# Performance work log

Measured on AMD Instinct MI355X. Metric: run time of the kernel, lower is better.

The kernel has to match this reference:

```python
import jax, jax.numpy as jnp
import numpy as np

C = 128
PC = 6
NH = 8
HD = C // NH
EPS = 1e-5


def _layernorm(x, g, b):
    m = jnp.mean(x, axis=-1, keepdims=True)
    v = jnp.mean((x - m) ** 2, axis=-1, keepdims=True)
    return (x - m) * jax.lax.rsqrt(v + EPS) * g + b


def setup_inputs() -> dict:
    key = jax.random.key(0)
    ks = jax.random.split(key, 16)
    s = 0.02
    inp = {
        "x": jax.random.normal(ks[0], (2, C, 32, 64, 64), dtype=jnp.float32),
        "polar_coords": jax.random.normal(ks[1], (2, PC, 32, 64, 64), dtype=jnp.float32),
        "Wq": jax.random.normal(ks[2], (C, C), dtype=jnp.float32) * s,
        "bq": jnp.zeros((C,), jnp.float32),
        "Wk": jax.random.normal(ks[3], (C, C), dtype=jnp.float32) * s,
        "bk": jnp.zeros((C,), jnp.float32),
        "Wv": jax.random.normal(ks[4], (C, C), dtype=jnp.float32) * s,
        "bv": jnp.zeros((C,), jnp.float32),
        "Wp": jax.random.normal(ks[5], (PC, C), dtype=jnp.float32) * s,
        "bp": jnp.zeros((C,), jnp.float32),
        "Wo": jax.random.normal(ks[6], (C, C), dtype=jnp.float32) * s,
        "bo": jnp.zeros((C,), jnp.float32),
        "g1": jnp.ones((C,), jnp.float32),
        "beta1": jnp.zeros((C,), jnp.float32),
        "g2": jnp.ones((C,), jnp.float32),
        "beta2": jnp.zeros((C,), jnp.float32),
        "W1": jax.random.normal(ks[7], (C, 4 * C), dtype=jnp.float32) * s,
        "bf1": jnp.zeros((4 * C,), jnp.float32),
        "W2": jax.random.normal(ks[8], (4 * C, C), dtype=jnp.float32) * s,
        "bf2": jnp.zeros((C,), jnp.float32),
    }
    return inp


def reference(x, polar_coords, Wq, bq, Wk, bk, Wv, bv, Wp, bp, Wo, bo,
              g1, beta1, g2, beta2, W1, bf1, W2, bf2):
    B, Cc, D, H, W = x.shape
    N = B * D * H * W
    # [B,C,D,H,W] -> [N,C]
    x_flat = jnp.transpose(x, (0, 2, 3, 4, 1)).reshape(N, Cc)
    polar_flat = jnp.transpose(polar_coords, (0, 2, 3, 4, 1)).reshape(N, -1)

    x_with_polar = x_flat + polar_flat @ Wp + bp
    residual = x_with_polar
    x_norm = _layernorm(x_with_polar, g1, beta1)

    Q = (x_norm @ Wq + bq).reshape(N, NH, HD)
    K = (x_norm @ Wk + bk).reshape(N, NH, HD)
    V = (x_norm @ Wv + bv).reshape(N, NH, HD)

    # tiny per-token cross-head attention: scores [N, NH, NH]
    scores = jnp.einsum('nhd,ngd->nhg', Q, K) / np.float32(np.sqrt(HD))
    attn = jax.nn.softmax(scores, axis=-1)
    attended = jnp.einsum('nhg,ngd->nhd', attn, V).reshape(N, Cc)

    out = attended @ Wo + bo + residual
    residual2 = out
    h = _layernorm(out, g2, beta2)
    h = jax.nn.relu(h @ W1 + bf1) @ W2 + bf2
    out = h + residual2

    out = out.reshape(B, D, H, W, Cc)
    return jnp.transpose(out, (0, 4, 1, 2, 3))
```

## Files before the change

kernel.cpp:

```cpp
#include <hip/hip_runtime.h>

typedef unsigned short u16;
typedef float f32x4 __attribute__((ext_vector_type(4)));
typedef short bf16x8 __attribute__((ext_vector_type(8)));

#define DHW 131072
#define OFF_WQ 0
#define OFF_WK 16384
#define OFF_WV 32768
#define OFF_WO 49152
#define OFF_W1 65536
#define OFF_W2 131072

__device__ __forceinline__ float b2f(u16 u){ union{unsigned i; float f;} x; x.i=((unsigned)u)<<16; return x.f; }
__device__ __forceinline__ u16 f2b(float f){ union{float f; unsigned u;} x; x.f=f; unsigned r=x.u+0x7fffu+((x.u>>16)&1u); return (u16)(r>>16); }
__device__ __forceinline__ int cofs(int tok, int cch){ return (tok<<7) + ((((cch>>3) ^ (tok&7)))<<3) + (cch&7); }

__global__ void pack_w(const float* __restrict__ Wq, const float* __restrict__ Wk,
                       const float* __restrict__ Wv, const float* __restrict__ Wo,
                       const float* __restrict__ W1, const float* __restrict__ W2,
                       u16* __restrict__ ws){
  int tid = blockIdx.x*256 + threadIdx.x;
  const float* src; int dst, K, N, fb;
  if      (tid <  2048){ src=Wq; dst=OFF_WQ; K=128; N=128; fb=tid;       }
  else if (tid <  4096){ src=Wk; dst=OFF_WK; K=128; N=128; fb=tid-2048;  }
  else if (tid <  6144){ src=Wv; dst=OFF_WV; K=128; N=128; fb=tid-4096;  }
  else if (tid <  8192){ src=Wo; dst=OFF_WO; K=128; N=128; fb=tid-6144;  }
  else if (tid < 16384){ src=W1; dst=OFF_W1; K=128; N=512; fb=tid-8192;  }
  else                 { src=W2; dst=OFF_W2; K=512; N=128; fb=tid-16384; }
  int l = fb & 63, f = fb >> 6;
  int ksc = K >> 5;
  int nt = f / ksc, ks = f - nt*ksc;
  int k0 = ks*32 + ((l>>4)<<3);
  int col = nt*16 + (l&15);
  union { uint4 v; u16 u[8]; } pk;
  #pragma unroll
  for (int j=0;j<8;j++) pk.u[j] = f2b(src[(k0+j)*N + col]);
  *reinterpret_cast<uint4*>(ws + dst + f*512 + l*8) = pk.v;
}

__device__ __forceinline__ void zacc(f32x4 (&a)[4][2]){
  #pragma unroll
  for (int i=0;i<4;i++){ a[i][0]=(f32x4){0.f,0.f,0.f,0.f}; a[i][1]=(f32x4){0.f,0.f,0.f,0.f}; }
}
__device__ __forceinline__ void mmT(const u16* __restrict__ act, const u16* __restrict__ wf,
                                    int ctb, int ksc, int ks0, int l, f32x4 (&acc)[4][2]){
  #pragma unroll
  for (int ks=0; ks<4; ++ks){
    bf16x8 w0 = *(const bf16x8*)(wf + ((ctb+0)*ksc + ks0+ks)*512 + l*8);
    bf16x8 w1 = *(const bf16x8*)(wf + ((ctb+1)*ksc + ks0+ks)*512 + l*8);
    int g = ks*4 + (l>>4);
    #pragma unroll
    for (int tt=0; tt<4; ++tt){
      int tok = tt*16 + (l&15);
      bf16x8 a = *(const bf16x8*)(act + (tok<<7) + ((g ^ (tok&7))<<3));
      acc[tt][0] = __builtin_amdgcn_mfma_f32_16x16x32_bf16(w0, a, acc[tt][0], 0,0,0);
      acc[tt][1] = __builtin_amdgcn_mfma_f32_16x16x32_bf16(w1, a, acc[tt][1], 0,0,0);
    }
  }
}
__device__ __forceinline__ void packT(ushort4 (&pk)[4][2], const f32x4 (&acc)[4][2],
                                      const u16* __restrict__ bias, int ctb, int l, bool relu){
  #pragma unroll
  for (int cw=0; cw<2; ++cw){
    int cch = (ctb+cw)*16 + ((l>>4)<<2);
    float b0=b2f(bias[cch]), b1=b2f(bias[cch+1]), b2v=b2f(bias[cch+2]), b3=b2f(bias[cch+3]);
    #pragma unroll
    for (int tt=0; tt<4; ++tt){
      float v0=acc[tt][cw][0]+b0, v1=acc[tt][cw][1]+b1, v2=acc[tt][cw][2]+b2v, v3=acc[tt][cw][3]+b3;
      if (relu){ v0=fmaxf(v0,0.f); v1=fmaxf(v1,0.f); v2=fmaxf(v2,0.f); v3=fmaxf(v3,0.f); }
      pk[tt][cw] = (ushort4){ f2b(v0), f2b(v1), f2b(v2), f2b(v3) };
    }
  }
}
__device__ __forceinline__ void storePK(u16* dst, const ushort4 (&pk)[4][2], int ctb, int l){
  #pragma unroll
  for (int cw=0; cw<2; ++cw){
    int cch = ((ctb+cw)*16 + ((l>>4)<<2)) & 127;
    #pragma unroll
    for (int tt=0; tt<4; ++tt){
      int tok = tt*16 + (l&15);
      *(ushort4*)&dst[cofs(tok,cch)] = pk[tt][cw];
    }
  }
}
__device__ __forceinline__ void load16(const u16* buf, int t, int c0, float* o){
  int g = c0 >> 3;
  union { uint4 v; u16 u[8]; } a, b;
  a.v = *(const uint4*)&buf[(t<<7) + (( g    ^ (t&7))<<3)];
  b.v = *(const uint4*)&buf[(t<<7) + (((g+1) ^ (t&7))<<3)];
  #pragma unroll
  for (int j=0;j<8;j++){ o[j]=b2f(a.u[j]); o[8+j]=b2f(b.u[j]); }
}

__global__ __launch_bounds__(256,4) void fused(
    const float* __restrict__ x, const float* __restrict__ pol,
    const float* __restrict__ Wp, const u16* __restrict__ ws,
    const float* __restrict__ bp, const float* __restrict__ bq,
    const float* __restrict__ bk, const float* __restrict__ bv,
    const float* __restrict__ bo, const float* __restrict__ bf1,
    const float* __restrict__ bf2, const float* __restrict__ g1,
    const float* __restrict__ be1, const float* __restrict__ g2,
    const float* __restrict__ be2, float* __restrict__ out)
{
  __shared__ __align__(16) unsigned char arena[40448];
  u16*   bufA = (u16*)  (arena);
  u16*   bufB = (u16*)  (arena + 16384);
  float* red   = (float*)(arena + 32768);
  float* stats = (float*)(arena + 34816);
  u16*   par   = (u16*)  (arena + 35328);

  const int tid = threadIdx.x;
  const int t   = tid & 63;
  const int p   = __builtin_amdgcn_readfirstlane(tid >> 6);
  const int l   = t;

  for (int i=tid; i<2560; i+=256){
    float v;
    if      (i< 128) v = bp [i];
    else if (i< 256) v = g1 [i-128];
    else if (i< 384) v = be1[i-256];
    else if (i< 512) v = g2 [i-384];
    else if (i< 640) v = be2[i-512];
    else if (i<1408) v = Wp [i-640];
    else if (i<1536) v = bq [i-1408];
    else if (i<1664) v = bk [i-1536];
    else if (i<1792) v = bv [i-1664];
    else if (i<1920) v = bo [i-1792];
    else if (i<2048) v = bf2[i-1920];
    else             v = bf1[i-2048];
    par[i] = f2b(v);
  }
  const int bi   = (int)((blockIdx.x*64) >> 17);
  const int dhw0 = (int)((blockIdx.x*64) & (DHW-1));
  const float* xb = x   + (size_t)bi*128*DHW + dhw0;
  const float* pb = pol + (size_t)bi*6*DHW + dhw0;
  float pl6[6];
  #pragma unroll
  for (int j=0;j<6;j++) pl6[j] = pb[(size_t)j*DHW + t];
  __syncthreads();

  float xp[32]; float s1=0.f, s2=0.f;
  #pragma unroll
  for (int it=0; it<32; ++it){
    int c = p*32 + it;
    float a = xb[(size_t)c*DHW + t] + b2f(par[c]);
    #pragma unroll
    for (int j=0;j<6;j++) a = fmaf(pl6[j], b2f(par[640 + j*128 + c]), a);
    xp[it]=a; s1+=a; s2+=a*a;
  }
  #pragma unroll
  for (int cl=0; cl<4; ++cl){
    union { uint4 v; u16 u[8]; } pk;
    #pragma unroll
    for (int j=0;j<8;j++) pk.u[j]=f2b(xp[cl*8+j]);
    *(uint4*)&bufB[(t<<7) + (((p*4+cl) ^ (t&7))<<3)] = pk.v;
  }
  red[p*64+t]=s1; red[256+p*64+t]=s2;
  __syncthreads();
  if (tid < 64){
    float a=0.f,b=0.f;
    #pragma unroll
    for (int i=0;i<4;i++){ a+=red[i*64+tid]; b+=red[256+i*64+tid]; }
    float m=a*0.0078125f, v=b*0.0078125f-m*m;
    stats[tid*2]=m; stats[tid*2+1]=rsqrtf(v+1e-5f);
  }
  __syncthreads();

  {
    float mn=stats[t*2], rs=stats[t*2+1];
    #pragma unroll
    for (int cl=0; cl<4; ++cl){
      union { uint4 v; u16 u[8]; } pk;
      #pragma unroll
      for (int j=0;j<8;j++){ int c=p*32+cl*8+j; pk.u[j]=f2b((xp[cl*8+j]-mn)*rs*b2f(par[128+c])+b2f(par[256+c])); }
      *(uint4*)&bufA[(t<<7) + (((p*4+cl) ^ (t&7))<<3)] = pk.v;
    }
  }
  ushort4 resq[4][2];
  #pragma unroll
  for (int cw=0; cw<2; ++cw){
    int cch = (p*2+cw)*16 + ((l>>4)<<2);
    #pragma unroll
    for (int tt=0; tt<4; ++tt) resq[tt][cw] = *(const ushort4*)&bufB[cofs(tt*16+(l&15), cch)];
  }
  __syncthreads();

  f32x4 acc[4][2]; ushort4 pkt[4][2];
  zacc(acc); mmT(bufA, ws+OFF_WQ, p*2, 4, 0, l, acc);
  packT(pkt, acc, par+1408, p*2, l, false); storePK(bufB, pkt, p*2, l);
  ushort4 pkV[4][2];
  zacc(acc); mmT(bufA, ws+OFF_WV, p*2, 4, 0, l, acc);
  packT(pkV, acc, par+1664, p*2, l, false);
  zacc(acc); mmT(bufA, ws+OFF_WK, p*2, 4, 0, l, acc);
  __syncthreads();
  packT(pkt, acc, par+1536, p*2, l, false); storePK(bufA, pkt, p*2, l);
  __syncthreads();

  float sc[16];
  {
    float qv[32];
    load16(bufB, t, p*32, qv); load16(bufB, t, p*32+16, qv+16);
    #pragma unroll
    for (int g8=0; g8<8; ++g8){
      float kv[16]; load16(bufA, t, g8*16, kv);
      float d0=0.f,d1=0.f;
      #pragma unroll
      for (int d=0; d<16; ++d){ d0=fmaf(qv[d],kv[d],d0); d1=fmaf(qv[16+d],kv[d],d1); }
      sc[g8]=d0*0.25f; sc[8+g8]=d1*0.25f;
    }
    #pragma unroll
    for (int hh=0; hh<2; ++hh){
      float mx = sc[hh*8];
      #pragma unroll
      for (int g8=1; g8<8; ++g8) mx = fmaxf(mx, sc[hh*8+g8]);
      float sm=0.f;
      #pragma unroll
      for (int g8=0; g8<8; ++g8){ float e=__expf(sc[hh*8+g8]-mx); sc[hh*8+g8]=e; sm+=e; }
      float inv = 1.f/sm;
      #pragma unroll
      for (int g8=0; g8<8; ++g8) sc[hh*8+g8]*=inv;
    }
  }
  __syncthreads();
  storePK(bufA, pkV, p*2, l);
  __syncthreads();
  {
    float ov[32];
    #pragma unroll
    for (int i=0;i<32;i++) ov[i]=0.f;
    #pragma unroll
    for (int g8=0; g8<8; ++g8){
      float vv[16]; load16(bufA, t, g8*16, vv);
      #pragma unroll
      for (int d=0; d<16; ++d){ ov[d]=fmaf(sc[g8],vv[d],ov[d]); ov[16+d]=fmaf(sc[8+g8],vv[d],ov[16+d]); }
    }
    #pragma unroll
    for (int cl=0; cl<4; ++cl){
      union { uint4 v; u16 u[8]; } pk;
      #pragma unroll
      for (int j=0;j<8;j++) pk.u[j]=f2b(ov[cl*8+j]);
      *(uint4*)&bufB[(t<<7) + (((p*4+cl) ^ (t&7))<<3)] = pk.v;
    }
  }
  __syncthreads();

  ushort4 res2q[4][2];
  zacc(acc); mmT(bufB, ws+OFF_WO, p*2, 4, 0, l, acc);
  #pragma unroll
  for (int cw=0; cw<2; ++cw){
    int cch = (p*2+cw)*16 + ((l>>4)<<2);
    float b0=b2f(par[1792+cch]), b1=b2f(par[1793+cch]), b2v=b2f(par[1794+cch]), b3=b2f(par[1795+cch]);
    #pragma unroll
    for (int tt=0; tt<4; ++tt){
      int tok = tt*16 + (l&15);
      ushort4 r4 = resq[tt][cw];
      ushort4 pk = (ushort4){ f2b(acc[tt][cw][0]+b0+b2f(r4.x)),
                              f2b(acc[tt][cw][1]+b1+b2f(r4.y)),
                              f2b(acc[tt][cw][2]+b2v+b2f(r4.z)),
                              f2b(acc[tt][cw][3]+b3+b2f(r4.w)) };
      res2q[tt][cw] = pk;
      *(ushort4*)&bufA[cofs(tok,cch)] = pk;
    }
  }
  __syncthreads();

  float ovl[32]; s1=0.f; s2=0.f;
  #pragma unroll
  for (int cl=0; cl<4; ++cl){
    union { uint4 v; u16 u[8]; } pk;
    pk.v = *(const uint4*)&bufA[(t<<7) + (((p*4+cl) ^ (t&7))<<3)];
    #pragma unroll
    for (int j=0;j<8;j++){ float v=b2f(pk.u[j]); ovl[cl*8+j]=v; s1+=v; s2+=v*v; }
  }
  red[p*64+t]=s1; red[256+p*64+t]=s2;
  __syncthreads();
  if (tid < 64){
    float a=0.f,b=0.f;
    #pragma unroll
    for (int i=0;i<4;i++){ a+=red[i*64+tid]; b+=red[256+i*64+tid]; }
    float m=a*0.0078125f, v=b*0.0078125f-m*m;
    stats[tid*2]=m; stats[tid*2+1]=rsqrtf(v+1e-5f);
  }
  __syncthreads();
  {
    float mn=stats[t*2], rs=stats[t*2+1];
    #pragma unroll
    for (int cl=0; cl<4; ++cl){
      union { uint4 v; u16 u[8]; } pk;
      #pragma unroll
      for (int j=0;j<8;j++){ int c=p*32+cl*8+j; pk.u[j]=f2b((ovl[cl*8+j]-mn)*rs*b2f(par[384+c])+b2f(par[512+c])); }
      *(uint4*)&bufB[(t<<7) + (((p*4+cl) ^ (t&7))<<3)] = pk.v;
    }
  }
  __syncthreads();

  f32x4 acc2[4][2]; zacc(acc2);
  #pragma unroll 1
  for (int ch=0; ch<4; ++ch){
    f32x4 acc1[4][2]; zacc(acc1);
    mmT(bufB, ws+OFF_W1, ch*8+p*2, 4, 0, l, acc1);
    packT(pkt, acc1, par+2048, ch*8+p*2, l, true); storePK(bufA, pkt, ch*8+p*2, l);
    __syncthreads();
    mmT(bufA, ws+OFF_W2, p*2, 16, ch*4, l, acc2);
    __syncthreads();
  }

  float* ob = out + (size_t)bi*128*DHW + dhw0;
  #pragma unroll
  for (int cw=0; cw<2; ++cw){
    int cch = (p*2+cw)*16 + ((l>>4)<<2);
    float b0=b2f(par[1920+cch]), b1=b2f(par[1921+cch]), b2v=b2f(par[1922+cch]), b3=b2f(par[1923+cch]);
    #pragma unroll
    for (int tt=0; tt<4; ++tt){
      int tok = tt*16 + (l&15);
      ushort4 r4 = res2q[tt][cw];
      ob[(size_t)(cch+0)*DHW + tok] = acc2[tt][cw][0] + b0 + b2f(r4.x);
      ob[(size_t)(cch+1)*DHW + tok] = acc2[tt][cw][1] + b1 + b2f(r4.y);
      ob[(size_t)(cch+2)*DHW + tok] = acc2[tt][cw][2] + b2v + b2f(r4.z);
      ob[(size_t)(cch+3)*DHW + tok] = acc2[tt][cw][3] + b3 + b2f(r4.w);
    }
  }
}

extern "C" void kernel_launch(void* const* d_in, const int* in_sizes, int n_in,
                              void* d_out, int out_size, void* d_ws, size_t ws_size,
                              hipStream_t stream){
  const float* x   = (const float*)d_in[0];
  const float* pol = (const float*)d_in[1];
  const float* Wq  = (const float*)d_in[2];
  const float* bq  = (const float*)d_in[3];
  const float* Wk  = (const float*)d_in[4];
  const float* bk  = (const float*)d_in[5];
  const float* Wv  = (const float*)d_in[6];
  const float* bv  = (const float*)d_in[7];
  const float* Wp  = (const float*)d_in[8];
  const float* bp  = (const float*)d_in[9];
  const float* Wo  = (const float*)d_in[10];
  const float* bo  = (const float*)d_in[11];
  const float* g1  = (const float*)d_in[12];
  const float* be1 = (const float*)d_in[13];
  const float* g2  = (const float*)d_in[14];
  const float* be2 = (const float*)d_in[15];
  const float* W1  = (const float*)d_in[16];
  const float* bf1 = (const float*)d_in[17];
  const float* W2  = (const float*)d_in[18];
  const float* bf2 = (const float*)d_in[19];
  u16* ws = (u16*)d_ws;
  pack_w<<<96, 256, 0, stream>>>(Wq, Wk, Wv, Wo, W1, W2, ws);
  fused<<<4096, 256, 0, stream>>>(x, pol, Wp, ws, bp, bq, bk, bv, bo, bf1, bf2,
                                  g1, be1, g2, be2, (float*)d_out);
}
```

Measured before the change: 469.9 us.

## Stage output through LDS for vectorized stores and use packed bf16 conversions

The final output is now written into shared memory as a channel-by-token tile (padded stride 68), then copied to global memory with 16-byte float4 stores per channel row, replacing scattered 4-byte stores. Scalar bf16 rounding is replaced by the v_cvt_pk_bf16_f32 instruction, and parameter loads from LDS are vectorized with cheap unpacking of bf16 pairs. The aim is to cut global store transactions and ALU work in the conversion-heavy sections. The cost is an extra barrier and 34 KB of LDS reused for staging, which overlays the existing buffers.

New measurement: 426.8 us. 1.1x faster.

```diff
diff --git a/kernel.cpp b/kernel.cpp
--- a/kernel.cpp
+++ b/kernel.cpp
@@ -14,6 +14,11 @@
 
 __device__ __forceinline__ float b2f(u16 u){ union{unsigned i; float f;} x; x.i=((unsigned)u)<<16; return x.f; }
 __device__ __forceinline__ u16 f2b(float f){ union{float f; unsigned u;} x; x.f=f; unsigned r=x.u+0x7fffu+((x.u>>16)&1u); return (u16)(r>>16); }
+__device__ __forceinline__ float blo(unsigned u){ union{unsigned i; float f;} x; x.i=u<<16; return x.f; }
+__device__ __forceinline__ float bhi(unsigned u){ union{unsigned i; float f;} x; x.i=u&0xffff0000u; return x.f; }
+__device__ __forceinline__ unsigned cvt2(float a, float b){
+  unsigned r; asm("v_cvt_pk_bf16_f32 %0, %1, %2" : "=v"(r) : "v"(a), "v"(b)); return r;
+}
 __device__ __forceinline__ int cofs(int tok, int cch){ return (tok<<7) + ((((cch>>3) ^ (tok&7)))<<3) + (cch&7); }
 
 __global__ void pack_w(const float* __restrict__ Wq, const float* __restrict__ Wk,
@@ -59,38 +64,41 @@
     }
   }
 }
-__device__ __forceinline__ void packT(ushort4 (&pk)[4][2], const f32x4 (&acc)[4][2],
+__device__ __forceinline__ void packT(uint2 (&pk)[4][2], const f32x4 (&acc)[4][2],
                                       const u16* __restrict__ bias, int ctb, int l, bool relu){
   #pragma unroll
   for (int cw=0; cw<2; ++cw){
     int cch = (ctb+cw)*16 + ((l>>4)<<2);
-    float b0=b2f(bias[cch]), b1=b2f(bias[cch+1]), b2v=b2f(bias[cch+2]), b3=b2f(bias[cch+3]);
+    uint2 bb = *(const uint2*)&bias[cch];
+    float b0=blo(bb.x), b1=bhi(bb.x), b2v=blo(bb.y), b3=bhi(bb.y);
     #pragma unroll
     for (int tt=0; tt<4; ++tt){
       float v0=acc[tt][cw][0]+b0, v1=acc[tt][cw][1]+b1, v2=acc[tt][cw][2]+b2v, v3=acc[tt][cw][3]+b3;
       if (relu){ v0=fmaxf(v0,0.f); v1=fmaxf(v1,0.f); v2=fmaxf(v2,0.f); v3=fmaxf(v3,0.f); }
-      pk[tt][cw] = (ushort4){ f2b(v0), f2b(v1), f2b(v2), f2b(v3) };
-    }
-  }
-}
-__device__ __forceinline__ void storePK(u16* dst, const ushort4 (&pk)[4][2], int ctb, int l){
+      uint2 q; q.x = cvt2(v0,v1); q.y = cvt2(v2,v3);
+      pk[tt][cw] = q;
+    }
+  }
+}
+__device__ __forceinline__ void storePK(u16* dst, const uint2 (&pk)[4][2], int ctb, int l){
   #pragma unroll
   for (int cw=0; cw<2; ++cw){
     int cch = ((ctb+cw)*16 + ((l>>4)<<2)) & 127;
     #pragma unroll
     for (int tt=0; tt<4; ++tt){
       int tok = tt*16 + (l&15);
-      *(ushort4*)&dst[cofs(tok,cch)] = pk[tt][cw];
+      *(uint2*)&dst[cofs(tok,cch)] = pk[tt][cw];
     }
   }
 }
 __device__ __forceinline__ void load16(const u16* buf, int t, int c0, float* o){
   int g = c0 >> 3;
-  union { uint4 v; u16 u[8]; } a, b;
-  a.v = *(const uint4*)&buf[(t<<7) + (( g    ^ (t&7))<<3)];
-  b.v = *(const uint4*)&buf[(t<<7) + (((g+1) ^ (t&7))<<3)];
-  #pragma unroll
-  for (int j=0;j<8;j++){ o[j]=b2f(a.u[j]); o[8+j]=b2f(b.u[j]); }
+  uint4 a = *(const uint4*)&buf[(t<<7) + (( g    ^ (t&7))<<3)];
+  uint4 b = *(const uint4*)&buf[(t<<7) + (((g+1) ^ (t&7))<<3)];
+  o[0]=blo(a.x); o[1]=bhi(a.x); o[2]=blo(a.y); o[3]=bhi(a.y);
+  o[4]=blo(a.z); o[5]=bhi(a.z); o[6]=blo(a.w); o[7]=bhi(a.w);
+  o[8]=blo(b.x); o[9]=bhi(b.x); o[10]=blo(b.y); o[11]=bhi(b.y);
+  o[12]=blo(b.z); o[13]=bhi(b.z); o[14]=blo(b.w); o[15]=bhi(b.w);
 }
 
 __global__ __launch_bounds__(256,4) void fused(
@@ -142,19 +150,33 @@
 
   float xp[32]; float s1=0.f, s2=0.f;
   #pragma unroll
-  for (int it=0; it<32; ++it){
-    int c = p*32 + it;
-    float a = xb[(size_t)c*DHW + t] + b2f(par[c]);
-    #pragma unroll
-    for (int j=0;j<6;j++) a = fmaf(pl6[j], b2f(par[640 + j*128 + c]), a);
-    xp[it]=a; s1+=a; s2+=a*a;
-  }
-  #pragma unroll
   for (int cl=0; cl<4; ++cl){
-    union { uint4 v; u16 u[8]; } pk;
-    #pragma unroll
-    for (int j=0;j<8;j++) pk.u[j]=f2b(xp[cl*8+j]);
-    *(uint4*)&bufB[(t<<7) + (((p*4+cl) ^ (t&7))<<3)] = pk.v;
+    int c0 = p*32 + cl*8;
+    uint4 bp4 = *(const uint4*)&par[c0];
+    float a0=xb[(size_t)(c0+0)*DHW + t]+blo(bp4.x);
+    float a1=xb[(size_t)(c0+1)*DHW + t]+bhi(bp4.x);
+    float a2=xb[(size_t)(c0+2)*DHW + t]+blo(bp4.y);
+    float a3=xb[(size_t)(c0+3)*DHW + t]+bhi(bp4.y);
+    float a4=xb[(size_t)(c0+4)*DHW + t]+blo(bp4.z);
+    float a5=xb[(size_t)(c0+5)*DHW + t]+bhi(bp4.z);
+    float a6=xb[(size_t)(c0+6)*DHW + t]+blo(bp4.w);
+    float a7=xb[(size_t)(c0+7)*DHW + t]+bhi(bp4.w);
+    #pragma unroll
+    for (int j=0;j<6;j++){
+      uint4 w4 = *(const uint4*)&par[640 + j*128 + c0];
+      float pj = pl6[j];
+      a0=fmaf(pj, blo(w4.x), a0); a1=fmaf(pj, bhi(w4.x), a1);
+      a2=fmaf(pj, blo(w4.y), a2); a3=fmaf(pj, bhi(w4.y), a3);
+      a4=fmaf(pj, blo(w4.z), a4); a5=fmaf(pj, bhi(w4.z), a5);
+      a6=fmaf(pj, blo(w4.w), a6); a7=fmaf(pj, bhi(w4.w), a7);
+    }
+    xp[cl*8+0]=a0; xp[cl*8+1]=a1; xp[cl*8+2]=a2; xp[cl*8+3]=a3;
+    xp[cl*8+4]=a4; xp[cl*8+5]=a5; xp[cl*8+6]=a6; xp[cl*8+7]=a7;
+    s1 += (a0+a1)+(a2+a3)+((a4+a5)+(a6+a7));
+    s2=fmaf(a0,a0,s2); s2=fmaf(a1,a1,s2); s2=fmaf(a2,a2,s2); s2=fmaf(a3,a3,s2);
+    s2=fmaf(a4,a4,s2); s2=fmaf(a5,a5,s2); s2=fmaf(a6,a6,s2); s2=fmaf(a7,a7,s2);
+    uint4 pk; pk.x=cvt2(a0,a1); pk.y=cvt2(a2,a3); pk.z=cvt2(a4,a5); pk.w=cvt2(a6,a7);
+    *(uint4*)&bufB[(t<<7) + (((p*4+cl) ^ (t&7))<<3)] = pk;
   }
   red[p*64+t]=s1; red[256+p*64+t]=s2;
   __syncthreads();
@@ -171,25 +193,34 @@
     float mn=stats[t*2], rs=stats[t*2+1];
     #pragma unroll
     for (int cl=0; cl<4; ++cl){
-      union { uint4 v; u16 u[8]; } pk;
-      #pragma unroll
-      for (int j=0;j<8;j++){ int c=p*32+cl*8+j; pk.u[j]=f2b((xp[cl*8+j]-mn)*rs*b2f(par[128+c])+b2f(par[256+c])); }
-      *(uint4*)&bufA[(t<<7) + (((p*4+cl) ^ (t&7))<<3)] = pk.v;
-    }
-  }
-  ushort4 resq[4][2];
+      int c0 = p*32 + cl*8;
+      uint4 g4 = *(const uint4*)&par[128+c0];
+      uint4 b4 = *(const uint4*)&par[256+c0];
+      float v0=(xp[cl*8+0]-mn)*rs*blo(g4.x)+blo(b4.x);
+      float v1=(xp[cl*8+1]-mn)*rs*bhi(g4.x)+bhi(b4.x);
+      float v2=(xp[cl*8+2]-mn)*rs*blo(g4.y)+blo(b4.y);
+      float v3=(xp[cl*8+3]-mn)*rs*bhi(g4.y)+bhi(b4.y);
+      float v4=(xp[cl*8+4]-mn)*rs*blo(g4.z)+blo(b4.z);
+      float v5=(xp[cl*8+5]-mn)*rs*bhi(g4.z)+bhi(b4.z);
+      float v6=(xp[cl*8+6]-mn)*rs*blo(g4.w)+blo(b4.w);
+      float v7=(xp[cl*8+7]-mn)*rs*bhi(g4.w)+bhi(b4.w);
+      uint4 pk; pk.x=cvt2(v0,v1); pk.y=cvt2(v2,v3); pk.z=cvt2(v4,v5); pk.w=cvt2(v6,v7);
+      *(uint4*)&bufA[(t<<7) + (((p*4+cl) ^ (t&7))<<3)] = pk;
+    }
+  }
+  uint2 resq[4][2];
   #pragma unroll
   for (int cw=0; cw<2; ++cw){
     int cch = (p*2+cw)*16 + ((l>>4)<<2);
     #pragma unroll
-    for (int tt=0; tt<4; ++tt) resq[tt][cw] = *(const ushort4*)&bufB[cofs(tt*16+(l&15), cch)];
-  }
-  __syncthreads();
-
-  f32x4 acc[4][2]; ushort4 pkt[4][2];
+    for (int tt=0; tt<4; ++tt) resq[tt][cw] = *(const uint2*)&bufB[cofs(tt*16+(l&15), cch)];
+  }
+  __syncthreads();
+
+  f32x4 acc[4][2]; uint2 pkt[4][2];
   zacc(acc); mmT(bufA, ws+OFF_WQ, p*2, 4, 0, l, acc);
   packT(pkt, acc, par+1408, p*2, l, false); storePK(bufB, pkt, p*2, l);
-  ushort4 pkV[4][2];
+  uint2 pkV[4][2];
   zacc(acc); mmT(bufA, ws+OFF_WV, p*2, 4, 0, l, acc);
   packT(pkV, acc, par+1664, p*2, l, false);
   zacc(acc); mmT(bufA, ws+OFF_WK, p*2, 4, 0, l, acc);
@@ -237,30 +268,32 @@
     }
     #pragma unroll
     for (int cl=0; cl<4; ++cl){
-      union { uint4 v; u16 u[8]; } pk;
-      #pragma unroll
-      for (int j=0;j<8;j++) pk.u[j]=f2b(ov[cl*8+j]);
-      *(uint4*)&bufB[(t<<7) + (((p*4+cl) ^ (t&7))<<3)] = pk.v;
-    }
-  }
-  __syncthreads();
-
-  ushort4 res2q[4][2];
+      uint4 pk;
+      pk.x=cvt2(ov[cl*8+0],ov[cl*8+1]); pk.y=cvt2(ov[cl*8+2],ov[cl*8+3]);
+      pk.z=cvt2(ov[cl*8+4],ov[cl*8+5]); pk.w=cvt2(ov[cl*8+6],ov[cl*8+7]);
+      *(uint4*)&bufB[(t<<7) + (((p*4+cl) ^ (t&7))<<3)] = pk;
+    }
+  }
+  __syncthreads();
+
+  uint2 res2q[4][2];
   zacc(acc); mmT(bufB, ws+OFF_WO, p*2, 4, 0, l, acc);
   #pragma unroll
   for (int cw=0; cw<2; ++cw){
     int cch = (p*2+cw)*16 + ((l>>4)<<2);
-    float b0=b2f(par[1792+cch]), b1=b2f(par[1793+cch]), b2v=b2f(par[1794+cch]), b3=b2f(par[1795+cch]);
+    uint2 bb = *(const uint2*)&par[1792+cch];
+    float b0=blo(bb.x), b1=bhi(bb.x), b2v=blo(bb.y), b3=bhi(bb.y);
     #pragma unroll
     for (int tt=0; tt<4; ++tt){
       int tok = tt*16 + (l&15);
-      ushort4 r4 = resq[tt][cw];
-      ushort4 pk = (ushort4){ f2b(acc[tt][cw][0]+b0+b2f(r4.x)),
-                              f2b(acc[tt][cw][1]+b1+b2f(r4.y)),
-                              f2b(acc[tt][cw][2]+b2v+b2f(r4.z)),
-                              f2b(acc[tt][cw][3]+b3+b2f(r4.w)) };
+      uint2 r = resq[tt][cw];
+      float v0 = acc[tt][cw][0]+b0+blo(r.x);
+      float v1 = acc[tt][cw][1]+b1+bhi(r.x);
+      float v2 = acc[tt][cw][2]+b2v+blo(r.y);
+      float v3 = acc[tt][cw][3]+b3+bhi(r.y);
+      uint2 pk; pk.x=cvt2(v0,v1); pk.y=cvt2(v2,v3);
       res2q[tt][cw] = pk;
-      *(ushort4*)&bufA[cofs(tok,cch)] = pk;
+      *(uint2*)&bufA[cofs(tok,cch)] = pk;
     }
   }
   __syncthreads();
@@ -268,10 +301,14 @@
   float ovl[32]; s1=0.f; s2=0.f;
   #pragma unroll
   for (int cl=0; cl<4; ++cl){
-    union { uint4 v; u16 u[8]; } pk;
-    pk.v = *(const uint4*)&bufA[(t<<7) + (((p*4+cl) ^ (t&7))<<3)];
-    #pragma unroll
-    for (int j=0;j<8;j++){ float v=b2f(pk.u[j]); ovl[cl*8+j]=v; s1+=v; s2+=v*v; }
+    uint4 pk = *(const uint4*)&bufA[(t<<7) + (((p*4+cl) ^ (t&7))<<3)];
+    float w0=blo(pk.x), w1=bhi(pk.x), w2=blo(pk.y), w3=bhi(pk.y);
+    float w4=blo(pk.z), w5=bhi(pk.z), w6=blo(pk.w), w7=bhi(pk.w);
+    ovl[cl*8+0]=w0; ovl[cl*8+1]=w1; ovl[cl*8+2]=w2; ovl[cl*8+3]=w3;
+    ovl[cl*8+4]=w4; ovl[cl*8+5]=w5; ovl[cl*8+6]=w6; ovl[cl*8+7]=w7;
+    s1 += (w0+w1)+(w2+w3)+((w4+w5)+(w6+w7));
+    s2=fmaf(w0,w0,s2); s2=fmaf(w1,w1,s2); s2=fmaf(w2,w2,s2); s2=fmaf(w3,w3,s2);
+    s2=fmaf(w4,w4,s2); s2=fmaf(w5,w5,s2); s2=fmaf(w6,w6,s2); s2=fmaf(w7,w7,s2);
   }
   red[p*64+t]=s1; red[256+p*64+t]=s2;
   __syncthreads();
@@ -287,10 +324,19 @@
     float mn=stats[t*2], rs=stats[t*2+1];
     #pragma unroll
     for (int cl=0; cl<4; ++cl){
-      union { uint4 v; u16 u[8]; } pk;
-      #pragma unroll
-      for (int j=0;j<8;j++){ int c=p*32+cl*8+j; pk.u[j]=f2b((ovl[cl*8+j]-mn)*rs*b2f(par[384+c])+b2f(par[512+c])); }
-      *(uint4*)&bufB[(t<<7) + (((p*4+cl) ^ (t&7))<<3)] = pk.v;
+      int c0 = p*32 + cl*8;
+      uint4 g4 = *(const uint4*)&par[384+c0];
+      uint4 b4 = *(const uint4*)&par[512+c0];
+      float v0=(ovl[cl*8+0]-mn)*rs*blo(g4.x)+blo(b4.x);
+      float v1=(ovl[cl*8+1]-mn)*rs*bhi(g4.x)+bhi(b4.x);
+      float v2=(ovl[cl*8+2]-mn)*rs*blo(g4.y)+blo(b4.y);
+      float v3=(ovl[cl*8+3]-mn)*rs*bhi(g4.y)+bhi(b4.y);
+      float v4=(ovl[cl*8+4]-mn)*rs*blo(g4.z)+blo(b4.z);
+      float v5=(ovl[cl*8+5]-mn)*rs*bhi(g4.z)+bhi(b4.z);
+      float v6=(ovl[cl*8+6]-mn)*rs*blo(g4.w)+blo(b4.w);
+      float v7=(ovl[cl*8+7]-mn)*rs*bhi(g4.w)+bhi(b4.w);
+      uint4 pk; pk.x=cvt2(v0,v1); pk.y=cvt2(v2,v3); pk.z=cvt2(v4,v5); pk.w=cvt2(v6,v7);
+      *(uint4*)&bufB[(t<<7) + (((p*4+cl) ^ (t&7))<<3)] = pk;
     }
   }
   __syncthreads();
@@ -306,20 +352,31 @@
     __syncthreads();
   }
 
-  float* ob = out + (size_t)bi*128*DHW + dhw0;
+  float* ostg = (float*)arena;
   #pragma unroll
   for (int cw=0; cw<2; ++cw){
     int cch = (p*2+cw)*16 + ((l>>4)<<2);
-    float b0=b2f(par[1920+cch]), b1=b2f(par[1921+cch]), b2v=b2f(par[1922+cch]), b3=b2f(par[1923+cch]);
+    uint2 bb = *(const uint2*)&par[1920+cch];
+    float b0=blo(bb.x), b1=bhi(bb.x), b2v=blo(bb.y), b3=bhi(bb.y);
     #pragma unroll
     for (int tt=0; tt<4; ++tt){
       int tok = tt*16 + (l&15);
-      ushort4 r4 = res2q[tt][cw];
-      ob[(size_t)(cch+0)*DHW + tok] = acc2[tt][cw][0] + b0 + b2f(r4.x);
-      ob[(size_t)(cch+1)*DHW + tok] = acc2[tt][cw][1] + b1 + b2f(r4.y);
-      ob[(size_t)(cch+2)*DHW + tok] = acc2[tt][cw][2] + b2v + b2f(r4.z);
-      ob[(size_t)(cch+3)*DHW + tok] = acc2[tt][cw][3] + b3 + b2f(r4.w);
-    }
+      uint2 r = res2q[tt][cw];
+      ostg[(cch+0)*68 + tok] = acc2[tt][cw][0] + b0  + blo(r.x);
+      ostg[(cch+1)*68 + tok] = acc2[tt][cw][1] + b1  + bhi(r.x);
+      ostg[(cch+2)*68 + tok] = acc2[tt][cw][2] + b2v + blo(r.y);
+      ostg[(cch+3)*68 + tok] = acc2[tt][cw][3] + b3  + bhi(r.y);
+    }
+  }
+  __syncthreads();
+  float* ob = out + (size_t)bi*128*DHW + dhw0;
+  #pragma unroll
+  for (int pass=0; pass<8; ++pass){
+    int i  = pass*256 + tid;
+    int c  = i >> 4;
+    int t4 = (i & 15) << 2;
+    f32x4 v = *(const f32x4*)&ostg[c*68 + t4];
+    *(f32x4*)&ob[(size_t)c*DHW + t4] = v;
   }
 }
 
```
